# Kernel tuning notes

Measured on AMD Instinct MI355X. Metric: run time of the kernel, lower is better.

Reference implementation:

```python
import jax, jax.numpy as jnp
import numpy as np

B, V, C, G, D, H, W, N = 1, 4, 32, 8, 8, 240, 320, 9
EPS = 1e-5  # BatchNorm3d default eps


def grid_sample(img, grid, align_corners, zeros_pad):
    # img [B,C,Hs,Ws], grid [B,Hg,Wg,2] normalized coords; mirrors torch F.grid_sample bilinear
    Bi, Ci, Hs, Ws = img.shape
    gx, gy = grid[..., 0], grid[..., 1]
    if align_corners:
        ix = (gx + 1.0) * 0.5 * (Ws - 1)
        iy = (gy + 1.0) * 0.5 * (Hs - 1)
    else:
        ix = ((gx + 1.0) * Ws - 1.0) * 0.5
        iy = ((gy + 1.0) * Hs - 1.0) * 0.5
    x0 = jnp.floor(ix)
    y0 = jnp.floor(iy)
    wx1 = ix - x0
    wy1 = iy - y0

    def corner(xi, yi, wgt):
        xc = jnp.clip(xi, 0, Ws - 1).astype(jnp.int32)
        yc = jnp.clip(yi, 0, Hs - 1).astype(jnp.int32)
        v = jax.vmap(lambda im, yy, xx: im[:, yy, xx])(img, yc, xc)  # [B,C,Hg,Wg]
        if zeros_pad:
            valid = ((xi >= 0) & (xi <= Ws - 1) & (yi >= 0) & (yi <= Hs - 1)).astype(img.dtype)
            wgt = wgt * valid
        return v * wgt[:, None]

    return (corner(x0, y0, (1 - wx1) * (1 - wy1)) + corner(x0 + 1, y0, wx1 * (1 - wy1))
            + corner(x0, y0 + 1, (1 - wx1) * wy1) + corner(x0 + 1, y0 + 1, wx1 * wy1))


def differentiable_warping(src_fea, src_proj, ref_proj, depth):
    # src_fea [B,Cf,H,W], projs [B,4,4], depth [B,D,H,W] -> [B,Cf,D,H,W]
    Bi, Cf, Hs, Ws = src_fea.shape
    Dd = depth.shape[1]
    proj = src_proj @ jnp.linalg.inv(ref_proj)
    rot, trans = proj[:, :3, :3], proj[:, :3, 3:4]
    yy, xx = jnp.meshgrid(jnp.arange(Hs, dtype=jnp.float32), jnp.arange(Ws, dtype=jnp.float32), indexing='ij')
    xyz = jnp.stack([xx.ravel(), yy.ravel(), jnp.ones(Hs * Ws, jnp.float32)], axis=0)  # [3,HW]
    rot_xyz = jnp.einsum('bij,jk->bik', rot, xyz)  # [B,3,HW]
    pxyz = rot_xyz[:, :, None, :] * depth.reshape(Bi, 1, Dd, Hs * Ws) + trans[:, :, :, None]  # [B,3,D,HW]
    neg = pxyz[:, 2] <= 1e-3
    px = jnp.where(neg, float(Ws), pxyz[:, 0])
    py = jnp.where(neg, float(Hs), pxyz[:, 1])
    pz = jnp.where(neg, 1.0, pxyz[:, 2])
    gx = (px / pz) / ((Ws - 1) / 2.0) - 1.0
    gy = (py / pz) / ((Hs - 1) / 2.0) - 1.0
    grid = jnp.stack([gx, gy], axis=-1).reshape(Bi, Dd * Hs, Ws, 2)
    grid = jax.lax.stop_gradient(grid)  # torch builds the warp grid under no_grad
    warped = grid_sample(src_fea, grid, align_corners=True, zeros_pad=True)  # [B,Cf,D*H,W]
    return warped.reshape(Bi, Cf, Dd, Hs, Ws)


def conv_bn_relu(x, w, bn):
    # 1x1x1 Conv3d (no bias) + BatchNorm3d (inference) + ReLU; x [B,Ci,D,H,W]
    y = jnp.einsum('oi,bidhw->bodhw', w, x)
    g, b, m, v = bn
    s = g / jnp.sqrt(v + EPS)
    return jax.nn.relu(y * s[:, None, None, None] + (b - m * s)[:, None, None, None])


def conv1(x, w, b):
    return jnp.einsum('oi,bidhw->bodhw', w, x) + b[:, None, None, None]


def pixel_wise_net(sim, w0, bn0, w1, bn1, w2, b2):
    y = conv_bn_relu(sim, w0, bn0)
    y = conv_bn_relu(y, w1, bn1)
    y = jax.nn.sigmoid(conv1(y, w2, b2))[:, 0]  # [B,D,H,W]
    return jnp.max(y, axis=1, keepdims=True)  # [B,1,H,W]


def _forward(ref_feature, src_features, ref_proj, src_projs, depth_sample, grid, weight,
             pw_w0, pw_bn0, pw_w1, pw_bn1, pw_w2, pw_b2,
             sn_w0, sn_bn0, sn_w1, sn_bn1, sn_w2, sn_b2):
    Bi, Cf, Hs, Ws = ref_feature.shape
    Gq = pw_w0.shape[1]
    Dd = depth_sample.shape[1]
    ref_g = ref_feature.reshape(Bi, Gq, Cf // Gq, 1, Hs, Ws)
    sim_sum = jnp.zeros((Bi, Gq, Dd, Hs, Ws), jnp.float32)
    w_sum = jnp.zeros((Bi, 1, 1, Hs, Ws), jnp.float32)
    vws = []
    for v in range(src_features.shape[0]):  # small fixed view count
        warped = differentiable_warping(src_features[v], src_projs[v], ref_proj, depth_sample)
        warped = warped.reshape(Bi, Gq, Cf // Gq, Dd, Hs, Ws)
        sim = jnp.mean(warped * ref_g, axis=2)  # [B,G,D,H,W] group correlation
        vw = pixel_wise_net(sim, pw_w0, pw_bn0, pw_w1, pw_bn1, pw_w2, pw_b2)  # [B,1,H,W]
        vws.append(vw)
        sim_sum = sim_sum + sim * vw[:, :, None]
        w_sum = w_sum + vw[:, :, None]
    x = sim_sum / w_sum
    # SimilarityNet: conv stack -> neighbor grid_sample -> adaptive weighted sum
    y = conv_bn_relu(x, sn_w0, sn_bn0)
    y = conv_bn_relu(y, sn_w1, sn_bn1)
    y = conv1(y, sn_w2, sn_b2)[:, 0]  # [B,D,H,W]
    s = grid_sample(y, grid, align_corners=False, zeros_pad=False)  # border pad, [B,D,N*H,W]
    Nn = grid.shape[1] // Hs
    s = s.reshape(Bi, Dd, Nn, Hs, Ws)
    score_vol = jnp.sum(s * weight, axis=2)  # [B,D,H,W]
    score = jax.nn.softmax(score_vol, axis=1)  # exp(log_softmax) == softmax
    depth = jnp.sum(depth_sample * score, axis=1)  # [B,H,W] (is_inverse=False)
    view_weights = jax.lax.stop_gradient(jnp.concatenate(vws, axis=1))  # [B,V,H,W]
    return depth, score, view_weights


def setup_inputs():
    key = jax.random.key(0)
    ks = jax.random.split(key, 20)
    ref_feature = jax.random.normal(ks[0], (B, C, H, W), jnp.float32)
    src_features = jax.random.normal(ks[1], (V, B, C, H, W), jnp.float32)
    f = 500.0
    K = np.array([[f, 0, W / 2.0, 0], [0, f, H / 2.0, 0], [0, 0, 1, 0], [0, 0, 0, 1]], np.float32)
    ref_proj = jnp.asarray(np.tile(K[None], (B, 1, 1)))
    sp = []
    for tx, ty in [(20.0, 0.0), (-20.0, 0.0), (0.0, 10.0), (0.0, -10.0)]:
        E = np.eye(4, dtype=np.float32)
        E[0, 3], E[1, 3] = tx, ty
        sp.append(np.tile((K @ E)[None], (B, 1, 1)))
    src_projs = jnp.asarray(np.stack(sp))
    depth_sample = jnp.sort(425.0 + 510.0 * jax.random.uniform(ks[2], (B, D, H, W), jnp.float32), axis=1)
    # evaluation neighbor grid: per-pixel +-3px learned-style offsets, align_corners=False normalization
    dx = jax.random.uniform(ks[3], (B, N, H, W), minval=-3.0, maxval=3.0)
    dy = jax.random.uniform(ks[4], (B, N, H, W), minval=-3.0, maxval=3.0)
    xs = jnp.arange(W, dtype=jnp.float32)[None, None, None, :]
    ys = jnp.arange(H, dtype=jnp.float32)[None, None, :, None]
    gx = (2.0 * (xs + dx) + 1.0) / W - 1.0
    gy = (2.0 * (ys + dy) + 1.0) / H - 1.0
    grid = jnp.stack([gx, gy], -1).reshape(B, N * H, W, 2)
    weight = jax.random.uniform(ks[5], (B, D, N, H, W), jnp.float32)  # feature*depth weight in (0,1)

    def bn(k, c):
        k1, k2, k3, k4 = jax.random.split(k, 4)
        return jnp.stack([1.0 + 0.1 * jax.random.normal(k1, (c,)), 0.1 * jax.random.normal(k2, (c,)),
                          0.01 * jax.random.normal(k3, (c,)), 1.0 + 0.1 * jax.random.uniform(k4, (c,))])

    return dict(ref_feature=ref_feature, src_features=src_features, ref_proj=ref_proj,
                src_projs=src_projs, depth_sample=depth_sample, grid=grid, weight=weight,
                pw_w0=0.1 * jax.random.normal(ks[6], (16, G)), pw_bn0=bn(ks[7], 16),
                pw_w1=0.1 * jax.random.normal(ks[8], (8, 16)), pw_bn1=bn(ks[9], 8),
                pw_w2=0.1 * jax.random.normal(ks[10], (1, 8)), pw_b2=jnp.zeros((1,), jnp.float32),
                sn_w0=0.1 * jax.random.normal(ks[11], (16, G)), sn_bn0=bn(ks[12], 16),
                sn_w1=0.1 * jax.random.normal(ks[13], (8, 16)), sn_bn1=bn(ks[14], 8),
                sn_w2=0.1 * jax.random.normal(ks[15], (1, 8)), sn_b2=jnp.zeros((1,), jnp.float32))


def reference(ref_feature, src_features, ref_proj, src_projs, depth_sample, grid, weight,
              pw_w0, pw_bn0, pw_w1, pw_bn1, pw_w2, pw_b2,
              sn_w0, sn_bn0, sn_w1, sn_bn1, sn_w2, sn_b2):
    return _forward(ref_feature, src_features, ref_proj, src_projs, depth_sample, grid, weight,
                    pw_w0, pw_bn0, pw_w1, pw_bn1, pw_w2, pw_b2,
                    sn_w0, sn_bn0, sn_w1, sn_bn1, sn_w2, sn_b2)
```

## Files before the change

### kernel.cpp

```cpp
#include <hip/hip_runtime.h>
#include <hip/hip_fp16.h>
#include <cstdint>
#include <cstddef>

#define HH 240
#define WW 320
#define HWPIX 76800
#define NVIEW 4
#define NCH 32
#define NGRP 8
#define NDEP 8
#define NNEI 9
#define QPLANE (HWPIX * 8)

#define OFF_TAB 64
#define OFF_Y    4096
#define OFF_SRCT 618496

typedef _Float16 h2 __attribute__((ext_vector_type(2)));
typedef __fp16  h8v __attribute__((ext_vector_type(8)));
typedef float f32x16 __attribute__((ext_vector_type(16)));

__device__ __forceinline__ float fdot2_(h2 a, h2 b, float c) {
#if __has_builtin(__builtin_amdgcn_fdot2)
  return __builtin_amdgcn_fdot2(a, b, c, false);
#else
  return c + (float)a.x * (float)b.x + (float)a.y * (float)b.y;
#endif
}
__device__ __forceinline__ h2 pk_(float a, float b) {
#if __has_builtin(__builtin_amdgcn_cvt_pkrtz)
  return __builtin_bit_cast(h2, __builtin_amdgcn_cvt_pkrtz(a, b));
#else
  h2 r; r.x = (_Float16)a; r.y = (_Float16)b; return r;
#endif
}
__device__ __forceinline__ float pkf_(float a, float b) {
  return __builtin_bit_cast(float, pk_(a, b));
}

__device__ __forceinline__ f32x16 mfma_(h8v a, h8v b, f32x16 c) {
  return __builtin_amdgcn_mfma_f32_32x32x16_f16(a, b, c, 0, 0, 0);
}

__device__ __forceinline__ float mlp_mfma(float4 x4, h8v w0f, h8v w1f,
                                          float4 b1s, float4 w2s, float b2v,
                                          bool lo) {
  f32x16 Z = {};
  float4 xsw;
  xsw.x = __shfl_xor(x4.x, 32, 64);
  xsw.y = __shfl_xor(x4.y, 32, 64);
  xsw.z = __shfl_xor(x4.z, 32, 64);
  xsw.w = __shfl_xor(x4.w, 32, 64);
  float4 cst;
  cst.x = __builtin_bit_cast(float, 0x00003C00u);
  cst.y = 0.0f; cst.z = 0.0f; cst.w = 0.0f;
  float4 blo, bhi;
  blo.x = lo ? x4.x : cst.x;  blo.y = lo ? x4.y : cst.y;
  blo.z = lo ? x4.z : cst.z;  blo.w = lo ? x4.w : cst.w;
  bhi.x = lo ? xsw.x : cst.x; bhi.y = lo ? xsw.y : cst.y;
  bhi.z = lo ? xsw.z : cst.z; bhi.w = lo ? xsw.w : cst.w;

  float yv0 = 0.0f, yv1 = 0.0f;
#pragma unroll
  for (int bb = 0; bb < 2; ++bb) {
    float4 bin = bb ? bhi : blo;
    f32x16 acc = mfma_(w0f, __builtin_bit_cast(h8v, bin), Z);
    float dw0 = pkf_(fmaxf(acc[0], 0.f), fmaxf(acc[1], 0.f));
    float dw1 = pkf_(fmaxf(acc[2], 0.f), fmaxf(acc[3], 0.f));
    float dw2 = pkf_(fmaxf(acc[4], 0.f), fmaxf(acc[5], 0.f));
    float dw3 = pkf_(fmaxf(acc[6], 0.f), fmaxf(acc[7], 0.f));
    float s0 = __shfl_xor(dw0, 32, 64);
    float s1 = __shfl_xor(dw1, 32, 64);
    float s2 = __shfl_xor(dw2, 32, 64);
    float s3 = __shfl_xor(dw3, 32, 64);
    float4 bf;
    bf.x = lo ? dw0 : s2;
    bf.y = lo ? dw1 : s3;
    bf.z = lo ? s0 : dw2;
    bf.w = lo ? s1 : dw3;
    f32x16 a2 = mfma_(w1f, __builtin_bit_cast(h8v, bf), Z);
    float p = fmaxf(a2[0] + b1s.x, 0.f) * w2s.x;
    p = fmaf(fmaxf(a2[1] + b1s.y, 0.f), w2s.y, p);
    p = fmaf(fmaxf(a2[2] + b1s.z, 0.f), w2s.z, p);
    p = fmaf(fmaxf(a2[3] + b1s.w, 0.f), w2s.w, p);
    p += __shfl_xor(p, 32, 64);
    if (bb) yv1 = p + b2v; else yv0 = p + b2v;
  }
  return lo ? yv0 : yv1;
}

__global__ __launch_bounds__(256) void k_prep(
    const float* __restrict__ src, const float* __restrict__ ref,
    __half* __restrict__ dst,
    const float* __restrict__ refP, const float* __restrict__ srcP,
    const float* __restrict__ pw0, const float* __restrict__ pbn0,
    const float* __restrict__ pw1, const float* __restrict__ pbn1,
    const float* __restrict__ pw2, const float* __restrict__ pb2,
    const float* __restrict__ sw0, const float* __restrict__ sbn0,
    const float* __restrict__ sw1, const float* __restrict__ sbn1,
    const float* __restrict__ sw2, const float* __restrict__ sb2,
    float* __restrict__ ws, int nTransBlocks) {
  if ((int)blockIdx.x == nTransBlocks) {
    int tid = threadIdx.x;
    if (tid < 128) {
      int net = tid >> 6;
      int l = tid & 63;
      int n = l & 31;
      int hi = l >> 5;
      const float* W0 = net ? sw0 : pw0;  const float* B0 = net ? sbn0 : pbn0;
      const float* W1 = net ? sw1 : pw1;  const float* B1 = net ? sbn1 : pbn1;
      const float* W2 = net ? sw2 : pw2;
      float* base = ws + OFF_TAB + net * 1024;
      float4 r;
      if (hi == 0 && n < 16) {
        float s = B0[n] / sqrtf(B0[48 + n] + 1e-5f) * 0.25f;
        r.x = pkf_(W0[n * 8 + 0] * s, W0[n * 8 + 1] * s);
        r.y = pkf_(W0[n * 8 + 2] * s, W0[n * 8 + 3] * s);
        r.z = pkf_(W0[n * 8 + 4] * s, W0[n * 8 + 5] * s);
        r.w = pkf_(W0[n * 8 + 6] * s, W0[n * 8 + 7] * s);
      } else if (hi == 1 && n < 16) {
        float s = B0[n] / sqrtf(B0[48 + n] + 1e-5f);
        float b0f = B0[16 + n] - B0[32 + n] * s;
        r.x = pkf_(b0f, 0.f); r.y = 0.f; r.z = 0.f; r.w = 0.f;
      } else { r.x = r.y = r.z = r.w = 0.f; }
      ((float4*)(base))[l] = r;
      float4 q;
      if (n < 8) {
        float s = B1[n] / sqrtf(B1[24 + n] + 1e-5f);
        int o = n * 16 + 8 * hi;
        q.x = pkf_(W1[o + 0] * s, W1[o + 1] * s);
        q.y = pkf_(W1[o + 2] * s, W1[o + 3] * s);
        q.z = pkf_(W1[o + 4] * s, W1[o + 5] * s);
        q.w = pkf_(W1[o + 6] * s, W1[o + 7] * s);
      } else { q.x = q.y = q.z = q.w = 0.f; }
      ((float4*)(base + 256))[l] = q;
      float4 b;
      {
        float bb[4];
        for (int rr = 0; rr < 4; ++rr) {
          int o = rr + 4 * hi;
          float s = B1[o] / sqrtf(B1[24 + o] + 1e-5f);
          bb[rr] = B1[8 + o] - B1[16 + o] * s;
        }
        b.x = bb[0]; b.y = bb[1]; b.z = bb[2]; b.w = bb[3];
      }
      ((float4*)(base + 512))[l] = b;
      float4 w2v;
      w2v.x = W2[0 + 4 * hi]; w2v.y = W2[1 + 4 * hi];
      w2v.z = W2[2 + 4 * hi]; w2v.w = W2[3 + 4 * hi];
      ((float4*)(base + 768))[l] = w2v;
    } else if (tid == 128) {
      ws[62] = pb2[0];
      ws[63] = sb2[0];
    } else if (tid == 129) {
      float a[4][8];
      for (int i = 0; i < 4; ++i)
        for (int j = 0; j < 4; ++j) { a[i][j] = refP[i * 4 + j]; a[i][4 + j] = (i == j) ? 1.0f : 0.0f; }
      for (int c = 0; c < 4; ++c) {
        int piv = c; float best = fabsf(a[c][c]);
        for (int r2 = c + 1; r2 < 4; ++r2) { float t = fabsf(a[r2][c]); if (t > best) { best = t; piv = r2; } }
        if (piv != c) for (int j = 0; j < 8; ++j) { float t = a[c][j]; a[c][j] = a[piv][j]; a[piv][j] = t; }
        float inv = 1.0f / a[c][c];
        for (int j = 0; j < 8; ++j) a[c][j] *= inv;
        for (int r2 = 0; r2 < 4; ++r2) if (r2 != c) {
          float f = a[r2][c];
          for (int j = 0; j < 8; ++j) a[r2][j] -= f * a[c][j];
        }
      }
      for (int v = 0; v < NVIEW; ++v) {
        const float* S = srcP + v * 16;
        for (int i = 0; i < 3; ++i)
          for (int j = 0; j < 4; ++j) {
            float p = S[i*4+0]*a[0][4+j] + S[i*4+1]*a[1][4+j] + S[i*4+2]*a[2][4+j] + S[i*4+3]*a[3][4+j];
            if (j < 3) ws[v * 12 + i * 3 + j] = p;
            else       ws[v * 12 + 9 + i] = p;
          }
      }
    }
    return;
  }
  int t = blockIdx.x * 256 + threadIdx.x;
  int vq = t / HWPIX;
  int pix = t - vq * HWPIX;
  int v = vq >> 2;
  int q = vq & 3;
  const float* s = (v < NVIEW) ? (src + ((size_t)(v * NCH + q * 8)) * HWPIX + pix)
                               : (ref + ((size_t)(q * 8)) * HWPIX + pix);
  union { h2 h[4]; float4 f; } u;
  u.h[0] = pk_(s[0],         s[HWPIX]);
  u.h[1] = pk_(s[2 * HWPIX], s[3 * HWPIX]);
  u.h[2] = pk_(s[4 * HWPIX], s[5 * HWPIX]);
  u.h[3] = pk_(s[6 * HWPIX], s[7 * HWPIX]);
  reinterpret_cast<float4*>(dst + (size_t)vq * QPLANE)[pix] = u.f;
}

__device__ __forceinline__ void tapq(const __half* __restrict__ p, float wtf,
                                     h2* __restrict__ wp, bool first) {
  _Float16 wh = (_Float16)wtf;
  h2 wt2 = h2{wh, wh};
  union { float4 f; h2 h[4]; } u;
  u.f = *reinterpret_cast<const float4*>(p);
#pragma unroll
  for (int c = 0; c < 4; ++c) {
    if (first) wp[c] = u.h[c] * wt2;
    else       wp[c] += u.h[c] * wt2;
  }
}

__global__ __launch_bounds__(512) void k_main(
    const __half* __restrict__ srcT, const float* __restrict__ depthS,
    const float* __restrict__ wsc,
    float* __restrict__ ybuf, float* __restrict__ outVW) {
  __shared__ float sred[NVIEW * NDEP * 64];
  int tid = threadIdx.x;
  int lane = tid & 63;
  int d = tid >> 6;
  bool lo = lane < 32;
  int bid = (int)blockIdx.x;
  int swz = (bid & 7) * 150 + (bid >> 3);
  int pix = swz * 64 + lane;
  int h = pix / WW;
  int w = pix - h * WW;
  float fx = (float)w, fy = (float)h;

  h8v w0f_pw = ((const h8v*)(wsc + OFF_TAB))[lane];
  h8v w1f_pw = ((const h8v*)(wsc + OFF_TAB + 256))[lane];
  float4 b1s_pw = ((const float4*)(wsc + OFF_TAB + 512))[lane];
  float4 w2s_pw = ((const float4*)(wsc + OFF_TAB + 768))[lane];
  float b2_pw = wsc[62];

  h2 rc[16];
  {
    const __half* refb = srcT + (size_t)16 * QPLANE;
#pragma unroll
    for (int q = 0; q < 4; ++q) {
      union { float4 f; h2 hh[4]; } u;
      u.f = *reinterpret_cast<const float4*>(refb + (size_t)q * QPLANE + (size_t)pix * 8);
      rc[4*q] = u.hh[0]; rc[4*q+1] = u.hh[1]; rc[4*q+2] = u.hh[2]; rc[4*q+3] = u.hh[3];
    }
  }
  float dep = depthS[d * HWPIX + pix];

  float4 xps[NVIEW];
  float scv[NVIEW];
#pragma unroll
  for (int v = 0; v < NVIEW; ++v) {
    const float* pr = wsc + v * 12;
    float rx = fmaf(pr[0], fx, fmaf(pr[1], fy, pr[2]));
    float ry = fmaf(pr[3], fx, fmaf(pr[4], fy, pr[5]));
    float rz = fmaf(pr[6], fx, fmaf(pr[7], fy, pr[8]));
    float pz_ = fmaf(rz, dep, pr[11]);
    bool neg = (pz_ <= 0.001f);
    float px_ = neg ? (float)WW : fmaf(rx, dep, pr[9]);
    float py_ = neg ? (float)HH : fmaf(ry, dep, pr[10]);
    float rpz = neg ? 1.0f : __fdividef(1.0f, pz_);
    float ix = px_ * rpz;
    float iy = py_ * rpz;
    float x0f = floorf(ix), y0f = floorf(iy);
    float wx1 = ix - x0f, wy1 = iy - y0f;
    float wx0 = 1.0f - wx1, wy0 = 1.0f - wy1;
    float x1f = x0f + 1.0f, y1f = y0f + 1.0f;
    float vx0 = (x0f >= 0.0f && x0f <= (float)(WW - 1)) ? 1.0f : 0.0f;
    float vx1 = (x1f >= 0.0f && x1f <= (float)(WW - 1)) ? 1.0f : 0.0f;
    float vy0 = (y0f >= 0.0f && y0f <= (float)(HH - 1)) ? 1.0f : 0.0f;
    float vy1 = (y1f >= 0.0f && y1f <= (float)(HH - 1)) ? 1.0f : 0.0f;
    int xa = (int)fminf(fmaxf(x0f, 0.0f), (float)(WW - 1));
    int xb = (int)fminf(fmaxf(x1f, 0.0f), (float)(WW - 1));
    int ya = (int)fminf(fmaxf(y0f, 0.0f), (float)(HH - 1));
    int yb = (int)fminf(fmaxf(y1f, 0.0f), (float)(HH - 1));
    float w00 = wx0 * wy0 * vx0 * vy0;
    float w01 = wx1 * wy0 * vx1 * vy0;
    float w10 = wx0 * wy1 * vx0 * vy1;
    float w11 = wx1 * wy1 * vx1 * vy1;

    int t00 = ya * WW + xa, t01 = ya * WW + xb;
    int t10 = yb * WW + xa, t11 = yb * WW + xb;

    float simf[NGRP];
    {
      const __half* vb = srcT + (size_t)(v * 4) * QPLANE;
      h2 wp[16];
#pragma unroll
      for (int q = 0; q < 4; ++q) {
        const __half* pb = vb + (size_t)q * QPLANE;
        tapq(pb + (size_t)t00 * 8, w00, wp + 4 * q, true);
        tapq(pb + (size_t)t01 * 8, w01, wp + 4 * q, false);
        tapq(pb + (size_t)t10 * 8, w10, wp + 4 * q, false);
        tapq(pb + (size_t)t11 * 8, w11, wp + 4 * q, false);
      }
#pragma unroll
      for (int g = 0; g < NGRP; ++g)
        simf[g] = fdot2_(wp[2*g+1], rc[2*g+1], fdot2_(wp[2*g], rc[2*g], 0.0f));
    }

    float4 xp;
    xp.x = pkf_(simf[0], simf[1]);
    xp.y = pkf_(simf[2], simf[3]);
    xp.z = pkf_(simf[4], simf[5]);
    xp.w = pkf_(simf[6], simf[7]);
    xps[v] = xp;
    scv[v] = mlp_mfma(xp, w0f_pw, w1f_pw, b1s_pw, w2s_pw, b2_pw, lo);
  }

#pragma unroll
  for (int v = 0; v < NVIEW; ++v) sred[(v << 9) | (d << 6) | lane] = scv[v];
  __syncthreads();

  float ssum[NGRP];
#pragma unroll
  for (int g = 0; g < NGRP; ++g) ssum[g] = 0.0f;
  float wsum = 0.0f;
#pragma unroll
  for (int v = 0; v < NVIEW; ++v) {
    float m = sred[(v << 9) | lane];
#pragma unroll
    for (int j = 1; j < NDEP; ++j) m = fmaxf(m, sred[(v << 9) | (j << 6) | lane]);
    float vw = __fdividef(1.0f, 1.0f + __expf(-m));
    h2 p0 = __builtin_bit_cast(h2, xps[v].x);
    h2 p1 = __builtin_bit_cast(h2, xps[v].y);
    h2 p2 = __builtin_bit_cast(h2, xps[v].z);
    h2 p3 = __builtin_bit_cast(h2, xps[v].w);
    ssum[0] = fmaf((float)p0.x, vw, ssum[0]);
    ssum[1] = fmaf((float)p0.y, vw, ssum[1]);
    ssum[2] = fmaf((float)p1.x, vw, ssum[2]);
    ssum[3] = fmaf((float)p1.y, vw, ssum[3]);
    ssum[4] = fmaf((float)p2.x, vw, ssum[4]);
    ssum[5] = fmaf((float)p2.y, vw, ssum[5]);
    ssum[6] = fmaf((float)p3.x, vw, ssum[6]);
    ssum[7] = fmaf((float)p3.y, vw, ssum[7]);
    wsum += vw;
    if (d == 0) outVW[v * HWPIX + pix] = vw;
  }

  float rw = __fdividef(1.0f, wsum);
  float4 xg;
  xg.x = pkf_(ssum[0] * rw, ssum[1] * rw);
  xg.y = pkf_(ssum[2] * rw, ssum[3] * rw);
  xg.z = pkf_(ssum[4] * rw, ssum[5] * rw);
  xg.w = pkf_(ssum[6] * rw, ssum[7] * rw);
  h8v w0f_sn = ((const h8v*)(wsc + OFF_TAB + 1024))[lane];
  h8v w1f_sn = ((const h8v*)(wsc + OFF_TAB + 1024 + 256))[lane];
  float4 b1s_sn = ((const float4*)(wsc + OFF_TAB + 1024 + 512))[lane];
  float4 w2s_sn = ((const float4*)(wsc + OFF_TAB + 1024 + 768))[lane];
  float b2_sn = wsc[63];
  float yv = mlp_mfma(xg, w0f_sn, w1f_sn, b1s_sn, w2s_sn, b2_sn, lo);
  ybuf[pix * NDEP + d] = yv;
}

__global__ __launch_bounds__(256) void k_score(
    const float* __restrict__ grid, const float* __restrict__ weight,
    const float* __restrict__ depthS, const float* __restrict__ ybuf,
    float* __restrict__ out) {
  int pix = blockIdx.x * 256 + threadIdx.x;
  int h = pix / WW;
  int w = pix - h * WW;
  float sv[NDEP];
#pragma unroll
  for (int d = 0; d < NDEP; ++d) sv[d] = 0.0f;

#pragma unroll 1
  for (int n = 0; n < NNEI; ++n) {
    int gi = ((n * HH + h) * WW + w) * 2;
    float gx = grid[gi], gy = grid[gi + 1];
    float ix = ((gx + 1.0f) * (float)WW - 1.0f) * 0.5f;
    float iy = ((gy + 1.0f) * (float)HH - 1.0f) * 0.5f;
    float x0f = floorf(ix), y0f = floorf(iy);
    float wx1 = ix - x0f, wy1 = iy - y0f;
    float wx0 = 1.0f - wx1, wy0 = 1.0f - wy1;
    int xa = (int)fminf(fmaxf(x0f, 0.0f), (float)(WW - 1));
    int xb = (int)fminf(fmaxf(x0f + 1.0f, 0.0f), (float)(WW - 1));
    int ya = (int)fminf(fmaxf(y0f, 0.0f), (float)(HH - 1));
    int yb2 = (int)fminf(fmaxf(y0f + 1.0f, 0.0f), (float)(HH - 1));
    const float4* p00 = reinterpret_cast<const float4*>(ybuf + (size_t)(ya * WW + xa) * NDEP);
    const float4* p01 = reinterpret_cast<const float4*>(ybuf + (size_t)(ya * WW + xb) * NDEP);
    const float4* p10 = reinterpret_cast<const float4*>(ybuf + (size_t)(yb2 * WW + xa) * NDEP);
    const float4* p11 = reinterpret_cast<const float4*>(ybuf + (size_t)(yb2 * WW + xb) * NDEP);
    float4 a00 = p00[0], b00 = p00[1];
    float4 a01 = p01[0], b01 = p01[1];
    float4 a10 = p10[0], b10 = p10[1];
    float4 a11 = p11[0], b11 = p11[1];
    const float* v00 = (const float*)&a00;
    const float* v01 = (const float*)&a01;
    const float* v10 = (const float*)&a10;
    const float* v11 = (const float*)&a11;
    const float* u00 = (const float*)&b00;
    const float* u01 = (const float*)&b01;
    const float* u10 = (const float*)&b10;
    const float* u11 = (const float*)&b11;
#pragma unroll
    for (int d = 0; d < NDEP; ++d) {
      float c00 = (d < 4) ? v00[d] : u00[d - 4];
      float c01 = (d < 4) ? v01[d] : u01[d - 4];
      float c10 = (d < 4) ? v10[d] : u10[d - 4];
      float c11 = (d < 4) ? v11[d] : u11[d - 4];
      float s = wy0 * fmaf(wx0, c00, wx1 * c01) + wy1 * fmaf(wx0, c10, wx1 * c11);
      float wn = weight[((size_t)(d * NNEI + n) * HH + h) * WW + w];
      sv[d] = fmaf(s, wn, sv[d]);
    }
  }
  float m = sv[0];
#pragma unroll
  for (int d = 1; d < NDEP; ++d) m = fmaxf(m, sv[d]);
  float e[NDEP], s8 = 0.0f;
#pragma unroll
  for (int d = 0; d < NDEP; ++d) { e[d] = __expf(sv[d] - m); s8 += e[d]; }
  float r = __fdividef(1.0f, s8);
  float dp = 0.0f;
#pragma unroll
  for (int d = 0; d < NDEP; ++d) {
    float sc = e[d] * r;
    out[HWPIX + d * HWPIX + pix] = sc;
    dp = fmaf(depthS[d * HWPIX + pix], sc, dp);
  }
  out[pix] = dp;
}

extern "C" void kernel_launch(void* const* d_in, const int* in_sizes, int n_in,
                              void* d_out, int out_size, void* d_ws, size_t ws_size,
                              hipStream_t stream) {
  const float* ref    = (const float*)d_in[0];
  const float* src    = (const float*)d_in[1];
  const float* refP   = (const float*)d_in[2];
  const float* srcP   = (const float*)d_in[3];
  const float* depthS = (const float*)d_in[4];
  const float* grid   = (const float*)d_in[5];
  const float* weight = (const float*)d_in[6];
  float* out = (float*)d_out;
  float* ws  = (float*)d_ws;
  __half* srcT = (__half*)(ws + OFF_SRCT);

  int transThreads = 20 * HWPIX;
  int nTransBlocks = transThreads / 256;

  k_prep<<<nTransBlocks + 1, 256, 0, stream>>>(
      src, ref, srcT, refP, srcP,
      (const float*)d_in[7],  (const float*)d_in[8],
      (const float*)d_in[9],  (const float*)d_in[10],
      (const float*)d_in[11], (const float*)d_in[12],
      (const float*)d_in[13], (const float*)d_in[14],
      (const float*)d_in[15], (const float*)d_in[16],
      (const float*)d_in[17], (const float*)d_in[18],
      ws, nTransBlocks);
  k_main<<<HWPIX / 64, 512, 0, stream>>>(srcT, depthS, ws, ws + OFF_Y, out + 9 * HWPIX);
  k_score<<<HWPIX / 256, 256, 0, stream>>>(grid, weight, depthS, ws + OFF_Y, out);
}
```

Baseline: 83.18 us.

## Process two depth planes per wave in k_main with 256-thread blocks

Each wave now handles two depth hypotheses (d and d+4) instead of one, so a block is 4 waves rather than 8. The per-view ray terms (rx, ry, rz), reference features and MLP weights are loaded or computed once and reused for both depths, and the view-weight max/sigmoid reduction is amortised over two outputs. It also gives more independent gather and MFMA work per thread for latency hiding. The cost is roughly doubled live registers, which may reduce occupancy, and fewer threads per block.

```diff
diff --git a/kernel.cpp b/kernel.cpp
--- a/kernel.cpp
+++ b/kernel.cpp
@@ -208,14 +208,72 @@
   }
 }
 
-__global__ __launch_bounds__(512) void k_main(
+__device__ __forceinline__ float4 view_sim(const __half* __restrict__ vb,
+                                           const h2* __restrict__ rc,
+                                           float rx, float ry, float rz,
+                                           float tx, float ty, float tz,
+                                           float dep) {
+  float pz_ = fmaf(rz, dep, tz);
+  bool neg = (pz_ <= 0.001f);
+  float px_ = neg ? (float)WW : fmaf(rx, dep, tx);
+  float py_ = neg ? (float)HH : fmaf(ry, dep, ty);
+  float rpz = neg ? 1.0f : __fdividef(1.0f, pz_);
+  float ix = px_ * rpz;
+  float iy = py_ * rpz;
+  float x0f = floorf(ix), y0f = floorf(iy);
+  float wx1 = ix - x0f, wy1 = iy - y0f;
+  float wx0 = 1.0f - wx1, wy0 = 1.0f - wy1;
+  float x1f = x0f + 1.0f, y1f = y0f + 1.0f;
+  float vx0 = (x0f >= 0.0f && x0f <= (float)(WW - 1)) ? 1.0f : 0.0f;
+  float vx1 = (x1f >= 0.0f && x1f <= (float)(WW - 1)) ? 1.0f : 0.0f;
+  float vy0 = (y0f >= 0.0f && y0f <= (float)(HH - 1)) ? 1.0f : 0.0f;
+  float vy1 = (y1f >= 0.0f && y1f <= (float)(HH - 1)) ? 1.0f : 0.0f;
+  int xa = (int)fminf(fmaxf(x0f, 0.0f), (float)(WW - 1));
+  int xb = (int)fminf(fmaxf(x1f, 0.0f), (float)(WW - 1));
+  int ya = (int)fminf(fmaxf(y0f, 0.0f), (float)(HH - 1));
+  int yb = (int)fminf(fmaxf(y1f, 0.0f), (float)(HH - 1));
+  float w00 = wx0 * wy0 * vx0 * vy0;
+  float w01 = wx1 * wy0 * vx1 * vy0;
+  float w10 = wx0 * wy1 * vx0 * vy1;
+  float w11 = wx1 * wy1 * vx1 * vy1;
+
+  int t00 = ya * WW + xa, t01 = ya * WW + xb;
+  int t10 = yb * WW + xa, t11 = yb * WW + xb;
+
+  h2 wp[16];
+#pragma unroll
+  for (int q = 0; q < 4; ++q) {
+    const __half* pb = vb + (size_t)q * QPLANE;
+    tapq(pb + (size_t)t00 * 8, w00, wp + 4 * q, true);
+    tapq(pb + (size_t)t01 * 8, w01, wp + 4 * q, false);
+    tapq(pb + (size_t)t10 * 8, w10, wp + 4 * q, false);
+    tapq(pb + (size_t)t11 * 8, w11, wp + 4 * q, false);
+  }
+  float s0 = fdot2_(wp[1], rc[1], fdot2_(wp[0], rc[0], 0.0f));
+  float s1 = fdot2_(wp[3], rc[3], fdot2_(wp[2], rc[2], 0.0f));
+  float s2 = fdot2_(wp[5], rc[5], fdot2_(wp[4], rc[4], 0.0f));
+  float s3 = fdot2_(wp[7], rc[7], fdot2_(wp[6], rc[6], 0.0f));
+  float s4 = fdot2_(wp[9], rc[9], fdot2_(wp[8], rc[8], 0.0f));
+  float s5 = fdot2_(wp[11], rc[11], fdot2_(wp[10], rc[10], 0.0f));
+  float s6 = fdot2_(wp[13], rc[13], fdot2_(wp[12], rc[12], 0.0f));
+  float s7 = fdot2_(wp[15], rc[15], fdot2_(wp[14], rc[14], 0.0f));
+  float4 xp;
+  xp.x = pkf_(s0, s1);
+  xp.y = pkf_(s2, s3);
+  xp.z = pkf_(s4, s5);
+  xp.w = pkf_(s6, s7);
+  return xp;
+}
+
+__global__ __launch_bounds__(256) void k_main(
     const __half* __restrict__ srcT, const float* __restrict__ depthS,
     const float* __restrict__ wsc,
     float* __restrict__ ybuf, float* __restrict__ outVW) {
   __shared__ float sred[NVIEW * NDEP * 64];
   int tid = threadIdx.x;
   int lane = tid & 63;
-  int d = tid >> 6;
+  int wv = tid >> 6;
+  int d0 = wv, d1 = wv + 4;
   bool lo = lane < 32;
   int bid = (int)blockIdx.x;
   int swz = (bid & 7) * 150 + (bid >> 3);
@@ -240,76 +298,36 @@
       rc[4*q] = u.hh[0]; rc[4*q+1] = u.hh[1]; rc[4*q+2] = u.hh[2]; rc[4*q+3] = u.hh[3];
     }
   }
-  float dep = depthS[d * HWPIX + pix];
-
-  float4 xps[NVIEW];
-  float scv[NVIEW];
+  float dep0 = depthS[d0 * HWPIX + pix];
+  float dep1 = depthS[d1 * HWPIX + pix];
+
+  float4 xps0[NVIEW], xps1[NVIEW];
+  float scv0[NVIEW], scv1[NVIEW];
 #pragma unroll
   for (int v = 0; v < NVIEW; ++v) {
     const float* pr = wsc + v * 12;
     float rx = fmaf(pr[0], fx, fmaf(pr[1], fy, pr[2]));
     float ry = fmaf(pr[3], fx, fmaf(pr[4], fy, pr[5]));
     float rz = fmaf(pr[6], fx, fmaf(pr[7], fy, pr[8]));
-    float pz_ = fmaf(rz, dep, pr[11]);
-    bool neg = (pz_ <= 0.001f);
-    float px_ = neg ? (float)WW : fmaf(rx, dep, pr[9]);
-    float py_ = neg ? (float)HH : fmaf(ry, dep, pr[10]);
-    float rpz = neg ? 1.0f : __fdividef(1.0f, pz_);
-    float ix = px_ * rpz;
-    float iy = py_ * rpz;
-    float x0f = floorf(ix), y0f = floorf(iy);
-    float wx1 = ix - x0f, wy1 = iy - y0f;
-    float wx0 = 1.0f - wx1, wy0 = 1.0f - wy1;
-    float x1f = x0f + 1.0f, y1f = y0f + 1.0f;
-    float vx0 = (x0f >= 0.0f && x0f <= (float)(WW - 1)) ? 1.0f : 0.0f;
-    float vx1 = (x1f >= 0.0f && x1f <= (float)(WW - 1)) ? 1.0f : 0.0f;
-    float vy0 = (y0f >= 0.0f && y0f <= (float)(HH - 1)) ? 1.0f : 0.0f;
-    float vy1 = (y1f >= 0.0f && y1f <= (float)(HH - 1)) ? 1.0f : 0.0f;
-    int xa = (int)fminf(fmaxf(x0f, 0.0f), (float)(WW - 1));
-    int xb = (int)fminf(fmaxf(x1f, 0.0f), (float)(WW - 1));
-    int ya = (int)fminf(fmaxf(y0f, 0.0f), (float)(HH - 1));
-    int yb = (int)fminf(fmaxf(y1f, 0.0f), (float)(HH - 1));
-    float w00 = wx0 * wy0 * vx0 * vy0;
-    float w01 = wx1 * wy0 * vx1 * vy0;
-    float w10 = wx0 * wy1 * vx0 * vy1;
-    float w11 = wx1 * wy1 * vx1 * vy1;
-
-    int t00 = ya * WW + xa, t01 = ya * WW + xb;
-    int t10 = yb * WW + xa, t11 = yb * WW + xb;
-
-    float simf[NGRP];
-    {
-      const __half* vb = srcT + (size_t)(v * 4) * QPLANE;
-      h2 wp[16];
-#pragma unroll
-      for (int q = 0; q < 4; ++q) {
-        const __half* pb = vb + (size_t)q * QPLANE;
-        tapq(pb + (size_t)t00 * 8, w00, wp + 4 * q, true);
-        tapq(pb + (size_t)t01 * 8, w01, wp + 4 * q, false);
-        tapq(pb + (size_t)t10 * 8, w10, wp + 4 * q, false);
-        tapq(pb + (size_t)t11 * 8, w11, wp + 4 * q, false);
-      }
-#pragma unroll
-      for (int g = 0; g < NGRP; ++g)
-        simf[g] = fdot2_(wp[2*g+1], rc[2*g+1], fdot2_(wp[2*g], rc[2*g], 0.0f));
-    }
-
-    float4 xp;
-    xp.x = pkf_(simf[0], simf[1]);
-    xp.y = pkf_(simf[2], simf[3]);
-    xp.z = pkf_(simf[4], simf[5]);
-    xp.w = pkf_(simf[6], simf[7]);
-    xps[v] = xp;
-    scv[v] = mlp_mfma(xp, w0f_pw, w1f_pw, b1s_pw, w2s_pw, b2_pw, lo);
-  }
-
-#pragma unroll
-  for (int v = 0; v < NVIEW; ++v) sred[(v << 9) | (d << 6) | lane] = scv[v];
+    const __half* vb = srcT + (size_t)(v * 4) * QPLANE;
+    float4 xp0 = view_sim(vb, rc, rx, ry, rz, pr[9], pr[10], pr[11], dep0);
+    float4 xp1 = view_sim(vb, rc, rx, ry, rz, pr[9], pr[10], pr[11], dep1);
+    xps0[v] = xp0;
+    xps1[v] = xp1;
+    scv0[v] = mlp_mfma(xp0, w0f_pw, w1f_pw, b1s_pw, w2s_pw, b2_pw, lo);
+    scv1[v] = mlp_mfma(xp1, w0f_pw, w1f_pw, b1s_pw, w2s_pw, b2_pw, lo);
+  }
+
+#pragma unroll
+  for (int v = 0; v < NVIEW; ++v) {
+    sred[(v << 9) | (d0 << 6) | lane] = scv0[v];
+    sred[(v << 9) | (d1 << 6) | lane] = scv1[v];
+  }
   __syncthreads();
 
-  float ssum[NGRP];
-#pragma unroll
-  for (int g = 0; g < NGRP; ++g) ssum[g] = 0.0f;
+  float ssum0[NGRP], ssum1[NGRP];
+#pragma unroll
+  for (int g = 0; g < NGRP; ++g) { ssum0[g] = 0.0f; ssum1[g] = 0.0f; }
   float wsum = 0.0f;
 #pragma unroll
   for (int v = 0; v < NVIEW; ++v) {
@@ -317,35 +335,53 @@
 #pragma unroll
     for (int j = 1; j < NDEP; ++j) m = fmaxf(m, sred[(v << 9) | (j << 6) | lane]);
     float vw = __fdividef(1.0f, 1.0f + __expf(-m));
-    h2 p0 = __builtin_bit_cast(h2, xps[v].x);
-    h2 p1 = __builtin_bit_cast(h2, xps[v].y);
-    h2 p2 = __builtin_bit_cast(h2, xps[v].z);
-    h2 p3 = __builtin_bit_cast(h2, xps[v].w);
-    ssum[0] = fmaf((float)p0.x, vw, ssum[0]);
-    ssum[1] = fmaf((float)p0.y, vw, ssum[1]);
-    ssum[2] = fmaf((float)p1.x, vw, ssum[2]);
-    ssum[3] = fmaf((float)p1.y, vw, ssum[3]);
-    ssum[4] = fmaf((float)p2.x, vw, ssum[4]);
-    ssum[5] = fmaf((float)p2.y, vw, ssum[5]);
-    ssum[6] = fmaf((float)p3.x, vw, ssum[6]);
-    ssum[7] = fmaf((float)p3.y, vw, ssum[7]);
+    h2 a0 = __builtin_bit_cast(h2, xps0[v].x);
+    h2 a1 = __builtin_bit_cast(h2, xps0[v].y);
+    h2 a2 = __builtin_bit_cast(h2, xps0[v].z);
+    h2 a3 = __builtin_bit_cast(h2, xps0[v].w);
+    ssum0[0] = fmaf((float)a0.x, vw, ssum0[0]);
+    ssum0[1] = fmaf((float)a0.y, vw, ssum0[1]);
+    ssum0[2] = fmaf((float)a1.x, vw, ssum0[2]);
+    ssum0[3] = fmaf((float)a1.y, vw, ssum0[3]);
+    ssum0[4] = fmaf((float)a2.x, vw, ssum0[4]);
+    ssum0[5] = fmaf((float)a2.y, vw, ssum0[5]);
+    ssum0[6] = fmaf((float)a3.x, vw, ssum0[6]);
+    ssum0[7] = fmaf((float)a3.y, vw, ssum0[7]);
+    h2 b0 = __builtin_bit_cast(h2, xps1[v].x);
+    h2 b1 = __builtin_bit_cast(h2, xps1[v].y);
+    h2 b2 = __builtin_bit_cast(h2, xps1[v].z);
+    h2 b3 = __builtin_bit_cast(h2, xps1[v].w);
+    ssum1[0] = fmaf((float)b0.x, vw, ssum1[0]);
+    ssum1[1] = fmaf((float)b0.y, vw, ssum1[1]);
+    ssum1[2] = fmaf((float)b1.x, vw, ssum1[2]);
+    ssum1[3] = fmaf((float)b1.y, vw, ssum1[3]);
+    ssum1[4] = fmaf((float)b2.x, vw, ssum1[4]);
+    ssum1[5] = fmaf((float)b2.y, vw, ssum1[5]);
+    ssum1[6] = fmaf((float)b3.x, vw, ssum1[6]);
+    ssum1[7] = fmaf((float)b3.y, vw, ssum1[7]);
     wsum += vw;
-    if (d == 0) outVW[v * HWPIX + pix] = vw;
+    if (wv == 0) outVW[v * HWPIX + pix] = vw;
   }
 
   float rw = __fdividef(1.0f, wsum);
-  float4 xg;
-  xg.x = pkf_(ssum[0] * rw, ssum[1] * rw);
-  xg.y = pkf_(ssum[2] * rw, ssum[3] * rw);
-  xg.z = pkf_(ssum[4] * rw, ssum[5] * rw);
-  xg.w = pkf_(ssum[6] * rw, ssum[7] * rw);
+  float4 xg0, xg1;
+  xg0.x = pkf_(ssum0[0] * rw, ssum0[1] * rw);
+  xg0.y = pkf_(ssum0[2] * rw, ssum0[3] * rw);
+  xg0.z = pkf_(ssum0[4] * rw, ssum0[5] * rw);
+  xg0.w = pkf_(ssum0[6] * rw, ssum0[7] * rw);
+  xg1.x = pkf_(ssum1[0] * rw, ssum1[1] * rw);
+  xg1.y = pkf_(ssum1[2] * rw, ssum1[3] * rw);
+  xg1.z = pkf_(ssum1[4] * rw, ssum1[5] * rw);
+  xg1.w = pkf_(ssum1[6] * rw, ssum1[7] * rw);
   h8v w0f_sn = ((const h8v*)(wsc + OFF_TAB + 1024))[lane];
   h8v w1f_sn = ((const h8v*)(wsc + OFF_TAB + 1024 + 256))[lane];
   float4 b1s_sn = ((const float4*)(wsc + OFF_TAB + 1024 + 512))[lane];
   float4 w2s_sn = ((const float4*)(wsc + OFF_TAB + 1024 + 768))[lane];
   float b2_sn = wsc[63];
-  float yv = mlp_mfma(xg, w0f_sn, w1f_sn, b1s_sn, w2s_sn, b2_sn, lo);
-  ybuf[pix * NDEP + d] = yv;
+  float yv0 = mlp_mfma(xg0, w0f_sn, w1f_sn, b1s_sn, w2s_sn, b2_sn, lo);
+  float yv1 = mlp_mfma(xg1, w0f_sn, w1f_sn, b1s_sn, w2s_sn, b2_sn, lo);
+  ybuf[pix * NDEP + d0] = yv0;
+  ybuf[pix * NDEP + d1] = yv1;
 }
 
 __global__ __launch_bounds__(256) void k_score(
@@ -442,6 +478,6 @@
       (const float*)d_in[15], (const float*)d_in[16],
       (const float*)d_in[17], (const float*)d_in[18],
       ws, nTransBlocks);
-  k_main<<<HWPIX / 64, 512, 0, stream>>>(srcT, depthS, ws, ws + OFF_Y, out + 9 * HWPIX);
+  k_main<<<HWPIX / 64, 256, 0, stream>>>(srcT, depthS, ws, ws + OFF_Y, out + 9 * HWPIX);
   k_score<<<HWPIX / 256, 256, 0, stream>>>(grid, weight, depthS, ws + OFF_Y, out);
 }
```

Measured after the change: 94.05 us. 13.1% more time.
